# Performance work log

Hardware: AMD Instinct MI355X
Metric: run time of the kernel (lower is better)

## Reference

```python
import jax, jax.numpy as jnp
import numpy as np

B = 1; D = 28; H = 28; W = 28; DIM = 192; HEADS = 6
WS = (7, 7, 7); SS = (3, 3, 3)
CH = DIM // HEADS
N = WS[0] * WS[1] * WS[2]
ND, NH, NWW = D // WS[0], H // WS[1], W // WS[2]
NW = ND * NH * NWW
L = D * H * W
HID = 4 * DIM


def _rel_pos_index():
    c = np.stack(np.meshgrid(np.arange(WS[0]), np.arange(WS[1]), np.arange(WS[2]), indexing='ij')).reshape(3, -1)
    r = (c[:, :, None] - c[:, None, :]).transpose(1, 2, 0)
    r[:, :, 0] += WS[0] - 1; r[:, :, 1] += WS[1] - 1; r[:, :, 2] += WS[2] - 1
    r[:, :, 0] *= (2 * WS[1] - 1) * (2 * WS[2] - 1)
    r[:, :, 1] *= 2 * WS[2] - 1
    return r.sum(-1).reshape(-1)

RPI = _rel_pos_index()  # (N*N,)


def _attn_mask():
    img = np.zeros((D, H, W), np.float32)
    cnt = 0
    sl = lambda w, s: (slice(0, -w), slice(-w, -s), slice(-s, None))
    for a in sl(WS[0], SS[0]):
        for bb in sl(WS[1], SS[1]):
            for cc in sl(WS[2], SS[2]):
                img[a, bb, cc] = cnt; cnt += 1
    mw = img.reshape(ND, WS[0], NH, WS[1], NWW, WS[2]).transpose(0, 2, 4, 1, 3, 5).reshape(-1, N)
    return np.where(mw[:, None, :] != mw[:, :, None], np.float32(-100.0), np.float32(0.0))

MASK = jnp.asarray(_attn_mask())  # (NW, N, N)


def ln(x, g, b):
    mu = x.mean(-1, keepdims=True)
    v = ((x - mu) ** 2).mean(-1, keepdims=True)
    return (x - mu) * jax.lax.rsqrt(v + 1e-5) * g + b


def conv3d(x, w, pad):
    return jax.lax.conv_general_dilated(x, w, (1, 1, 1), [(pad, pad)] * 3,
                                        dimension_numbers=('NCDHW', 'OIDHW', 'NCDHW'))


def bn3d(x, g, b):
    mu = x.mean((0, 2, 3, 4), keepdims=True)
    var = x.var((0, 2, 3, 4), keepdims=True)
    return (x - mu) * jax.lax.rsqrt(var + 1e-5) * g.reshape(1, -1, 1, 1, 1) + b.reshape(1, -1, 1, 1, 1)


def offset_block(x, w1, g1, b1, w2, g2, b2, w3):
    x = jax.nn.relu(bn3d(conv3d(x, w1, 1), g1, b1))
    x = jax.nn.relu(bn3d(conv3d(x, w2, 1), g2, b2))
    return conv3d(x, w3, 0)  # (B, 3*HEADS, D, H, W)


def warp(vol, flow):
    # vol: (B,HEADS,CH,D,H,W), flow: (B,HEADS,3,D,H,W) voxel displacements; trilinear, border-clamped
    gd, gh, gw = jnp.meshgrid(jnp.arange(D, dtype=jnp.float32), jnp.arange(H, dtype=jnp.float32),
                              jnp.arange(W, dtype=jnp.float32), indexing='ij')
    cd = jnp.clip(gd + flow[:, :, 0], 0.0, D - 1)
    chh = jnp.clip(gh + flow[:, :, 1], 0.0, H - 1)
    cw = jnp.clip(gw + flow[:, :, 2], 0.0, W - 1)
    d0 = jnp.floor(cd).astype(jnp.int32); d1 = jnp.minimum(d0 + 1, D - 1)
    h0 = jnp.floor(chh).astype(jnp.int32); h1 = jnp.minimum(h0 + 1, H - 1)
    w0 = jnp.floor(cw).astype(jnp.int32); w1 = jnp.minimum(w0 + 1, W - 1)
    fd = (cd - d0).reshape(B, HEADS, 1, -1)
    fh = (chh - h0).reshape(B, HEADS, 1, -1)
    fw = (cw - w0).reshape(B, HEADS, 1, -1)
    vf = vol.reshape(B, HEADS, CH, -1)
    def gat(di, hi, wi):
        idx = ((di * H + hi) * W + wi).reshape(B, HEADS, 1, -1)
        return jnp.take_along_axis(vf, idx, axis=3)
    out = (gat(d0, h0, w0) * (1 - fd) * (1 - fh) * (1 - fw)
           + gat(d0, h0, w1) * (1 - fd) * (1 - fh) * fw
           + gat(d0, h1, w0) * (1 - fd) * fh * (1 - fw)
           + gat(d0, h1, w1) * (1 - fd) * fh * fw
           + gat(d1, h0, w0) * fd * (1 - fh) * (1 - fw)
           + gat(d1, h0, w1) * fd * (1 - fh) * fw
           + gat(d1, h1, w0) * fd * fh * (1 - fw)
           + gat(d1, h1, w1) * fd * fh * fw)
    return out.reshape(B, HEADS, CH, D, H, W)


def win_part(x):  # (B,D,H,W,C) -> (B*NW, N, C)
    c = x.shape[-1]
    x = x.reshape(B, ND, WS[0], NH, WS[1], NWW, WS[2], c)
    return x.transpose(0, 1, 3, 5, 2, 4, 6, 7).reshape(B * NW, N, c)


def dwin_part(x):  # (B,HEADS,D,H,W,CH) -> (B*NW, N, DIM)
    x = x.reshape(B, HEADS, ND, WS[0], NH, WS[1], NWW, WS[2], CH)
    x = x.transpose(0, 2, 4, 6, 3, 5, 7, 1, 8)
    return x.reshape(B * NW, N, DIM)


def win_rev(x):  # (B*NW, N, DIM) -> (B,D,H,W,DIM)
    x = x.reshape(B, ND, NH, NWW, WS[0], WS[1], WS[2], DIM)
    return x.transpose(0, 1, 4, 2, 5, 3, 6, 7).reshape(B, D, H, W, DIM)


def kv(x, w, b):
    y = (x @ w.T + b).reshape(x.shape[0], N, 2, HEADS, CH).transpose(2, 0, 3, 1, 4)
    return y[0], y[1]


def to_heads(x):
    return x.reshape(x.shape[0], N, HEADS, CH).transpose(0, 2, 1, 3)


def _forward(mov, fix, norm1_g, norm1_b, offm_w1, offm_g1, offm_b1, offm_w2, offm_g2, offm_b2, offm_w3, offf_w1, offf_g1, offf_b1, offf_w2, offf_g2, offf_b2, offf_w3, mq_w, mq_b, mkv_w, mkv_b, fq_w, fq_b, fkv_w, fkv_b, mproj_w, mproj_b, fproj_w, fproj_b, rpb_table, norm2_g, norm2_b, fc1_w, fc1_b, fc2_w, fc2_b):
    m = ln(mov, norm1_g, norm1_b).reshape(B, D, H, W, DIM)
    f = ln(fix, norm1_g, norm1_b).reshape(B, D, H, W, DIM)
    off_m = offset_block(jnp.concatenate([m, f], -1).transpose(0, 4, 1, 2, 3), offm_w1, offm_g1, offm_b1, offm_w2, offm_g2, offm_b2, offm_w3)
    off_f = offset_block(jnp.concatenate([f, m], -1).transpose(0, 4, 1, 2, 3), offf_w1, offf_g1, offf_b1, offf_w2, offf_g2, offf_b2, offf_w3)
    mh = m.transpose(0, 4, 1, 2, 3).reshape(B, HEADS, CH, D, H, W)
    fh = f.transpose(0, 4, 1, 2, 3).reshape(B, HEADS, CH, D, H, W)
    dmov = warp(mh, off_m.reshape(B, HEADS, 3, D, H, W)).transpose(0, 1, 3, 4, 5, 2)  # (B,h,D,H,W,c)
    dfix = warp(fh, off_f.reshape(B, HEADS, 3, D, H, W)).transpose(0, 1, 3, 4, 5, 2)
    sh = (-SS[0], -SS[1], -SS[2])
    mw_ = win_part(jnp.roll(m, sh, (1, 2, 3)))
    fw_ = win_part(jnp.roll(f, sh, (1, 2, 3)))
    dmw = dwin_part(jnp.roll(dmov, sh, (2, 3, 4)))
    dfw = dwin_part(jnp.roll(dfix, sh, (2, 3, 4)))
    B_ = B * NW
    scale = CH ** -0.5
    mK, mV = kv(mw_, mkv_w, mkv_b)
    fK, fV = kv(fw_, fkv_w, fkv_b)
    dmQ = to_heads(dmw @ mq_w.T + mq_b) * scale
    dfQ = to_heads(dfw @ fq_w.T + fq_b) * scale
    rpb = rpb_table[RPI].reshape(N, N, HEADS).transpose(2, 0, 1)  # (HEADS,N,N)
    def attend(q, k, v):
        a = jnp.einsum('bhnc,bhmc->bhnm', q, k) + rpb[None]
        a = (a.reshape(B, NW, HEADS, N, N) + MASK[None, :, None]).reshape(B_, HEADS, N, N)
        a = jax.nn.softmax(a, axis=-1)
        return jnp.einsum('bhnm,bhmc->bhnc', a, v).transpose(0, 2, 1, 3).reshape(B_, N, DIM)
    mo = attend(dfQ, mK, mV) @ mproj_w.T + mproj_b
    fo = attend(dmQ, fK, fV) @ fproj_w.T + fproj_b
    mo = jnp.roll(win_rev(mo), SS, (1, 2, 3)).reshape(B, L, DIM)
    fo = jnp.roll(win_rev(fo), SS, (1, 2, 3)).reshape(B, L, DIM)
    m_out = mov + mo
    f_out = fix + fo
    def mlp(x):
        return jax.nn.gelu(x @ fc1_w.T + fc1_b, approximate=False) @ fc2_w.T + fc2_b
    m_out = m_out + mlp(ln(m_out, norm2_g, norm2_b))
    f_out = f_out + mlp(ln(f_out, norm2_g, norm2_b))
    return jnp.stack([m_out, f_out])  # (2, B, L, DIM)


def setup_inputs():
    key = jax.random.key(0)
    ks = iter(jax.random.split(key, 64))
    nrm = lambda shape, s=0.02: jax.random.normal(next(ks), shape, jnp.float32) * s
    d = {}
    d['mov'] = jax.random.normal(next(ks), (B, L, DIM), jnp.float32)
    d['fix'] = jax.random.normal(next(ks), (B, L, DIM), jnp.float32)
    d['norm1_g'] = jnp.ones((DIM,)); d['norm1_b'] = jnp.zeros((DIM,))
    for p in ('offm', 'offf'):
        d[p + '_w1'] = nrm((DIM, 2 * DIM, 3, 3, 3))
        d[p + '_g1'] = jnp.ones((DIM,)); d[p + '_b1'] = jnp.zeros((DIM,))
        d[p + '_w2'] = nrm((DIM // 2, DIM, 3, 3, 3))
        d[p + '_g2'] = jnp.ones((DIM // 2,)); d[p + '_b2'] = jnp.zeros((DIM // 2,))
        d[p + '_w3'] = nrm((3 * HEADS, DIM // 2, 1, 1, 1))
    for p, o in (('mq_w', DIM), ('mkv_w', 2 * DIM), ('fq_w', DIM), ('fkv_w', 2 * DIM), ('mproj_w', DIM), ('fproj_w', DIM)):
        d[p] = nrm((o, DIM))
    for p, o in (('mq_b', DIM), ('mkv_b', 2 * DIM), ('fq_b', DIM), ('fkv_b', 2 * DIM), ('mproj_b', DIM), ('fproj_b', DIM)):
        d[p] = jnp.zeros((o,))
    d['rpb_table'] = nrm(((2 * WS[0] - 1) * (2 * WS[1] - 1) * (2 * WS[2] - 1), HEADS))
    d['norm2_g'] = jnp.ones((DIM,)); d['norm2_b'] = jnp.zeros((DIM,))
    d['fc1_w'] = nrm((HID, DIM)); d['fc1_b'] = jnp.zeros((HID,))
    d['fc2_w'] = nrm((DIM, HID)); d['fc2_b'] = jnp.zeros((DIM,))
    return d


def reference(mov, fix, norm1_g, norm1_b, offm_w1, offm_g1, offm_b1, offm_w2, offm_g2, offm_b2, offm_w3, offf_w1, offf_g1, offf_b1, offf_w2, offf_g2, offf_b2, offf_w3, mq_w, mq_b, mkv_w, mkv_b, fq_w, fq_b, fkv_w, fkv_b, mproj_w, mproj_b, fproj_w, fproj_b, rpb_table, norm2_g, norm2_b, fc1_w, fc1_b, fc2_w, fc2_b):
    return _forward(mov, fix, norm1_g, norm1_b, offm_w1, offm_g1, offm_b1, offm_w2, offm_g2, offm_b2, offm_w3, offf_w1, offf_g1, offf_b1, offf_w2, offf_g2, offf_b2, offf_w3, mq_w, mq_b, mkv_w, mkv_b, fq_w, fq_b, fkv_w, fkv_b, mproj_w, mproj_b, fproj_w, fproj_b, rpb_table, norm2_g, norm2_b, fc1_w, fc1_b, fc2_w, fc2_b)
```

## Files before the change

### kernel.cpp

```cpp
#include <hip/hip_runtime.h>

#define LTOT 21952
#define NTOK 343

typedef unsigned short u16;
typedef unsigned int   u32;
typedef __attribute__((ext_vector_type(8))) short short8;
typedef __attribute__((ext_vector_type(4))) float float4v;

__device__ __forceinline__ u16 f2b(float f){
  u32 x = __float_as_uint(f);
  u32 r = (x + 0x7fffu + ((x>>16)&1u)) >> 16;
  return (u16)r;
}

__global__ __launch_bounds__(64) void k_ln(const float* __restrict__ mov, const float* __restrict__ fix,
                                           const float* __restrict__ g, const float* __restrict__ b,
                                           float* __restrict__ om, float* __restrict__ of){
  int row = blockIdx.x;
  const float* src; float* dst;
  if (row < LTOT){ src = mov + (size_t)row*192; dst = om + (size_t)row*192; }
  else          { src = fix + (size_t)(row-LTOT)*192; dst = of + (size_t)(row-LTOT)*192; }
  int t = threadIdx.x;
  float x0 = src[t], x1 = src[t+64], x2 = src[t+128];
  float s = x0+x1+x2, s2 = x0*x0 + x1*x1 + x2*x2;
  for (int o=32;o;o>>=1){ s += __shfl_xor(s,o); s2 += __shfl_xor(s2,o); }
  float mu = s*(1.f/192.f);
  float var = s2*(1.f/192.f) - mu*mu;
  float rs = rsqrtf(var + 1e-5f);
  dst[t]     = (x0-mu)*rs*g[t]     + b[t];
  dst[t+64]  = (x1-mu)*rs*g[t+64]  + b[t+64];
  dst[t+128] = (x2-mu)*rs*g[t+128] + b[t+128];
}

__global__ __launch_bounds__(64) void k_ln1(const float* __restrict__ x,
                                            const float* __restrict__ g, const float* __restrict__ b,
                                            float* __restrict__ y){
  int row = blockIdx.x;
  const float* src = x + (size_t)row*192;
  float* dst = y + (size_t)row*192;
  int t = threadIdx.x;
  float x0 = src[t], x1 = src[t+64], x2 = src[t+128];
  float s = x0+x1+x2, s2 = x0*x0 + x1*x1 + x2*x2;
  for (int o=32;o;o>>=1){ s += __shfl_xor(s,o); s2 += __shfl_xor(s2,o); }
  float mu = s*(1.f/192.f);
  float var = s2*(1.f/192.f) - mu*mu;
  float rs = rsqrtf(var + 1e-5f);
  dst[t]     = (x0-mu)*rs*g[t]     + b[t];
  dst[t+64]  = (x1-mu)*rs*g[t+64]  + b[t+64];
  dst[t+128] = (x2-mu)*rs*g[t+128] + b[t+128];
}

__global__ void k_prepw1b(const float* __restrict__ src, u16* __restrict__ dst, int swap){
  int idx = blockIdx.x*256 + threadIdx.x;
  if (idx >= 192*10368) return;
  int n = idx / 10368; int k = idx - n*10368;
  int t = k / 384; int c = k - t*384;
  int cs = c + swap; if (cs >= 384) cs -= 384;
  dst[idx] = f2b(src[((size_t)n*384 + cs)*27 + t]);
}
__global__ void k_prepw2b(const float* __restrict__ src, u16* __restrict__ dst){
  int idx = blockIdx.x*256 + threadIdx.x;
  if (idx >= 96*5184) return;
  int n = idx / 5184; int k = idx - n*5184;
  int t = k / 192; int c = k - t*192;
  dst[idx] = f2b(src[((size_t)n*192 + c)*27 + t]);
}
__global__ void k_prepwb(const float* __restrict__ src, u16* __restrict__ dst, int count){
  int idx = blockIdx.x*256 + threadIdx.x;
  if (idx < count) dst[idx] = f2b(src[idx]);
}

__global__ void k_prepbias(const float* __restrict__ rpt, float* __restrict__ bm){
  int idx = blockIdx.x*256 + threadIdx.x;
  if (idx >= 48*123904) return;
  int th = idx / 123904; int r = idx - th*123904;
  int key = r / 352; int q = r - key*352;
  int type = th / 6; int h = th - type*6;
  float v;
  if (key >= 343 || q >= 343){
    v = -30000.f;
  } else {
    int ki = key/49, kj = (key/7)%7, kk = key%7;
    int qi = q/49,   qj = (q/7)%7,   qk = q%7;
    int ridx = ((qi-ki+6)*13 + (qj-kj+6))*13 + (qk-kk+6);
    float rv = rpt[ridx*6 + h];
    int bd = (type>>2)&1, bh = (type>>1)&1, bw = type&1;
    int lq_ = (bd?((qi<4)?1:2):0)*9 + (bh?((qj<4)?1:2):0)*3 + (bw?((qk<4)?1:2):0);
    int lk_ = (bd?((ki<4)?1:2):0)*9 + (bh?((kj<4)?1:2):0)*3 + (bw?((kk<4)?1:2):0);
    v = rv + ((lq_==lk_) ? 0.f : -100.f);
  }
  bm[idx] = v;
}

__global__ __launch_bounds__(192) void k_pad1(const float* __restrict__ m_, const float* __restrict__ f_,
                                              u16* __restrict__ xp){
  int p = blockIdx.x; int t = threadIdx.x;
  int pd = p/900; int r = p - pd*900; int ph = r/30; int pw = r - ph*30;
  int d = pd-1, h = ph-1, w = pw-1;
  u16 vm = 0, vf = 0;
  if ((unsigned)d < 28u && (unsigned)h < 28u && (unsigned)w < 28u){
    size_t l = (size_t)((d*28+h)*28+w)*192 + t;
    vm = f2b(m_[l]); vf = f2b(f_[l]);
  }
  xp[(size_t)p*384 + t] = vm;
  xp[(size_t)p*384 + 192 + t] = vf;
}
__global__ __launch_bounds__(192) void k_pad2(const float* __restrict__ t1,
                                              const float* __restrict__ a1, const float* __restrict__ b1,
                                              u16* __restrict__ xp2){
  int p = blockIdx.x; int t = threadIdx.x;
  int pd = p/900; int r = p - pd*900; int ph = r/30; int pw = r - ph*30;
  int d = pd-1, h = ph-1, w = pw-1;
  u16 v = 0;
  if ((unsigned)d < 28u && (unsigned)h < 28u && (unsigned)w < 28u){
    float xv = t1[(size_t)((d*28+h)*28+w)*192 + t];
    v = f2b(fmaxf(xv*a1[t] + b1[t], 0.f));
  }
  xp2[(size_t)p*192 + t] = v;
}

template<int CIN, int COUT>
__global__ __launch_bounds__(256, 4) void k_convmfma(const u16* __restrict__ xpA,
                                                     const u16* __restrict__ xpB,
                                                     const u16* __restrict__ wA,
                                                     const u16* __restrict__ wB,
                                                     float* __restrict__ outA,
                                                     float* __restrict__ outB){
  constexpr int K = 27*CIN;
  constexpr int CH = CIN/32;
  constexpr int STEPS = 27*CH;
  constexpr int NT = COUT/32;
  constexpr int NB8 = COUT/32;
  __shared__ __align__(16) u16 As[2][64*40];
  __shared__ __align__(16) u16 Bs[2][COUT*40];
  int tid = threadIdx.x;
  int b0 = blockIdx.x;
  int xcd = b0 & 7, ii = b0 >> 3;
  int bid = (xcd < 6 ? xcd*86 : 516 + (xcd-6)*85) + ii;
  int which = (bid >= 343) ? 1 : 0;
  int t = bid - which*343;
  const u16* xp  = which ? xpB : xpA;
  const u16* wtb = which ? wB : wA;
  float* out = which ? outB : outA;
  int v0 = t*64;
  int sv  = tid>>2;
  int c8u = (tid&3)*8;
  int av = v0 + sv;
  int d = av/784; int rm2 = av - d*784; int hh = rm2/28; int ww = rm2 - hh*28;
  int pbase = (d*30 + hh)*30 + ww;
  int lane = tid&63, wv = tid>>6;
  int lm = lane&15, lq = lane>>4;
  int mbase = (wv>>1)*32;
  int nbase = (wv&1)*(COUT/2);

  float4v acc[2][NT];
  #pragma unroll
  for (int mt=0; mt<2; mt++)
    #pragma unroll
    for (int nt=0; nt<NT; nt++) acc[mt][nt] = (float4v)0.f;

  uint4 a_r;
  uint2 b_r[NB8];
  auto load_s = [&](int s){
    int tp = s/CH, cc = s - tp*CH;
    int td = tp/9, tr = tp - td*9, th = tr/3, tw = tr - th*3;
    int toff = td*900 + th*30 + tw;
    a_r = *(const uint4*)(xp + (size_t)(pbase + toff)*CIN + cc*32 + c8u);
    #pragma unroll
    for (int j=0;j<NB8;j++){
      int bi = tid + j*256;
      int n = bi>>3, c4 = (bi&7)*4;
      b_r[j] = *(const uint2*)(wtb + (size_t)n*K + s*32 + c4);
    }
  };
  auto write_s = [&](int buf){
    *(uint4*)(&As[buf][sv*40 + c8u]) = a_r;
    #pragma unroll
    for (int j=0;j<NB8;j++){
      int bi = tid + j*256;
      int n = bi>>3, c4 = (bi&7)*4;
      *(uint2*)(&Bs[buf][n*40 + c4]) = b_r[j];
    }
  };

  load_s(0);
  write_s(0);
  __syncthreads();
  for (int s = 0; s < STEPS; s++){
    if (s+1 < STEPS) load_s(s+1);
    int buf = s&1;
    short8 aa[2], bb[NT];
    #pragma unroll
    for (int mt=0; mt<2; mt++)
      aa[mt] = *(const short8*)(&As[buf][(mbase + mt*16 + lm)*40 + lq*8]);
    #pragma unroll
    for (int nt=0; nt<NT; nt++)
      bb[nt] = *(const short8*)(&Bs[buf][(nbase + nt*16 + lm)*40 + lq*8]);
    #pragma unroll
    for (int nt=0; nt<NT; nt++)
      #pragma unroll
      for (int mt=0; mt<2; mt++)
        acc[mt][nt] = __builtin_amdgcn_mfma_f32_16x16x32_bf16(aa[mt], bb[nt], acc[mt][nt], 0, 0, 0);
    if (s+1 < STEPS) write_s((s+1)&1);
    __syncthreads();
  }
  #pragma unroll
  for (int mt=0; mt<2; mt++)
    #pragma unroll
    for (int nt=0; nt<NT; nt++)
      #pragma unroll
      for (int r=0; r<4; r++){
        int row = v0 + mbase + mt*16 + lq*4 + r;
        int col = nbase + nt*16 + lm;
        out[(size_t)row*COUT + col] = acc[mt][nt][r];
      }
}

template<int K, int NF, int GATHER, int ASRC, int EPI>
__global__ __launch_bounds__(256) void k_gemm(const float* __restrict__ Af,
                                              const u16* __restrict__ Ab,
                                              const u16* __restrict__ B,
                                              const float* __restrict__ bias,
                                              const float* __restrict__ resid,
                                              float* __restrict__ outf,
                                              u16* __restrict__ out16,
                                              u16* __restrict__ out16b,
                                              float scale){
  constexpr int STEPS = K/32;
  constexpr int NB = NF/64;
  __shared__ __align__(16) u16 As[2][64*40];
  __shared__ __align__(16) u16 Bs[2][64*40];
  __shared__ int map[64];
  int tid = threadIdx.x;
  int bid = blockIdx.x;
  int mb = bid / NB, nb = bid - mb*NB;
  int v0 = mb*64, ncol0 = nb*64;
  if (tid < 64){
    int r = v0 + tid;
    int src;
    if (GATHER == 0){
      src = r;
    } else if (GATHER == 1){
      int w = r/343; int n = r - w*343;
      int nd = w>>4, nh = (w>>2)&3, nw = w&3;
      int i = n/49; int rr = n - i*49; int j = rr/7; int k2 = rr - j*7;
      int dd = nd*7 + i + 3; if (dd >= 28) dd -= 28;
      int hh = nh*7 + j + 3; if (hh >= 28) hh -= 28;
      int ww = nw*7 + k2 + 3; if (ww >= 28) ww -= 28;
      src = (dd*28 + hh)*28 + ww;
    } else {
      int l = r;
      int d = l/784; int rm = l - d*784; int y = rm/28; int x = rm - y*28;
      int dp = d-3; if (dp<0) dp+=28;
      int yp = y-3; if (yp<0) yp+=28;
      int xq = x-3; if (xq<0) xq+=28;
      int nd = dp/7, i = dp - nd*7;
      int nh = yp/7, j = yp - nh*7;
      int nw = xq/7, k2 = xq - nw*7;
      src = ((nd*4+nh)*4+nw)*NTOK + (i*7+j)*7 + k2;
    }
    map[tid] = src;
  }
  __syncthreads();
  int sv = tid>>2, c8 = (tid&3)*8;
  int arow = map[sv];
  int lane = tid&63, wv = tid>>6;
  int lm = lane&15, lq = lane>>4;
  int mbase = (wv>>1)*32, nbase = (wv&1)*32;

  float4v acc[2][2];
  #pragma unroll
  for (int mt=0; mt<2; mt++)
    #pragma unroll
    for (int nt=0; nt<2; nt++) acc[mt][nt] = (float4v)0.f;

  float4 afr0, afr1; uint4 abr; uint4 bvr;
  auto load_s = [&](int s){
    if (ASRC == 0){
      const float* ap = Af + (size_t)arow*K + s*32 + c8;
      afr0 = *(const float4*)ap;
      afr1 = *(const float4*)(ap+4);
    } else {
      abr = *(const uint4*)(Ab + (size_t)arow*K + s*32 + c8);
    }
    bvr = *(const uint4*)(B + (size_t)(ncol0 + sv)*K + s*32 + c8);
  };
  auto write_s = [&](int buf){
    if (ASRC == 0){
      uint4 pk;
      pk.x = (u32)f2b(afr0.x) | ((u32)f2b(afr0.y)<<16);
      pk.y = (u32)f2b(afr0.z) | ((u32)f2b(afr0.w)<<16);
      pk.z = (u32)f2b(afr1.x) | ((u32)f2b(afr1.y)<<16);
      pk.w = (u32)f2b(afr1.z) | ((u32)f2b(afr1.w)<<16);
      *(uint4*)(&As[buf][sv*40 + c8]) = pk;
    } else {
      *(uint4*)(&As[buf][sv*40 + c8]) = abr;
    }
    *(uint4*)(&Bs[buf][sv*40 + c8]) = bvr;
  };

  load_s(0);
  write_s(0);
  __syncthreads();
  for (int s = 0; s < STEPS; s++){
    if (s+1 < STEPS) load_s(s+1);
    int buf = s&1;
    short8 aa[2], bb[2];
    #pragma unroll
    for (int mt=0; mt<2; mt++)
      aa[mt] = *(const short8*)(&As[buf][(mbase + mt*16 + lm)*40 + lq*8]);
    #pragma unroll
    for (int nt=0; nt<2; nt++)
      bb[nt] = *(const short8*)(&Bs[buf][(nbase + nt*16 + lm)*40 + lq*8]);
    #pragma unroll
    for (int nt=0; nt<2; nt++)
      #pragma unroll
      for (int mt=0; mt<2; mt++)
        acc[mt][nt] = __builtin_amdgcn_mfma_f32_16x16x32_bf16(aa[mt], bb[nt], acc[mt][nt], 0, 0, 0);
    if (s+1 < STEPS) write_s((s+1)&1);
    __syncthreads();
  }
  float bv[2];
  #pragma unroll
  for (int nt=0; nt<2; nt++) bv[nt] = bias ? bias[ncol0 + nbase + nt*16 + lm] : 0.f;
  #pragma unroll
  for (int mt=0; mt<2; mt++){
    #pragma unroll
    for (int r=0; r<4; r++){
      int row = v0 + mbase + mt*16 + lq*4 + r;
      if (EPI == 0 || EPI == 3){
        int w = row/343; int tok = row - w*343;
        #pragma unroll
        for (int nt=0; nt<2; nt++){
          int col = ncol0 + nbase + nt*16 + lm;
          float val = (acc[mt][nt][r] + bv[nt]) * scale;
          if (EPI == 0){
            int h = col>>5, c = col&31;
            out16[((size_t)(w*6 + h)*343 + tok)*32 + c] = f2b(val);
          } else {
            u16* dst = (col < 192) ? out16 : out16b;
            int cc = (col < 192) ? col : col - 192;
            int h = cc>>5, c = cc&31;
            dst[((size_t)(w*6 + h)*343 + tok)*32 + c] = f2b(val);
          }
        }
      } else if (EPI == 1){
        #pragma unroll
        for (int nt=0; nt<2; nt++){
          int col = ncol0 + nbase + nt*16 + lm;
          size_t o = (size_t)row*NF + col;
          outf[o] = acc[mt][nt][r] + bv[nt] + resid[o];
        }
      } else {
        #pragma unroll
        for (int nt=0; nt<2; nt++){
          int col = ncol0 + nbase + nt*16 + lm;
          float v = acc[mt][nt][r] + bv[nt];
          float gl = 0.5f*v*(1.f + erff(v*0.70710678118f));
          out16[(size_t)row*NF + col] = f2b(gl);
        }
      }
    }
  }
}

__global__ __launch_bounds__(192) void k_bnsum(const float* __restrict__ x, int C,
                                               float* __restrict__ psum){
  int bid = blockIdx.x, t = threadIdx.x;
  int rpi = 192/C;
  int c  = (C==192) ? t : (t % 96);
  int ro = (C==192) ? 0 : (t / 96);
  float s=0.f, s2=0.f;
  int base = bid*343;
  for (int r = ro; r < 343; r += rpi){
    float v = x[(size_t)(base+r)*C + c];
    s += v; s2 += v*v;
  }
  psum[(size_t)bid*384 + t]       = s;
  psum[(size_t)bid*384 + 192 + t] = s2;
}
__global__ void k_bnfin(const float* __restrict__ psum, int C,
                        const float* __restrict__ g, const float* __restrict__ b,
                        float* __restrict__ a_out, float* __restrict__ b_out){
  int c = threadIdx.x;
  if (c >= C) return;
  int slots = 192/C;
  float s=0.f, s2=0.f;
  for (int bb=0; bb<64; bb++)
    for (int k=0; k<slots; k++){
      s  += psum[(size_t)bb*384 + k*C + c];
      s2 += psum[(size_t)bb*384 + 192 + k*C + c];
    }
  float mu = s/(float)LTOT;
  float var = s2/(float)LTOT - mu*mu;
  float rstd = rsqrtf(var + 1e-5f);
  float aa = rstd * g[c];
  a_out[c] = aa;
  b_out[c] = b[c] - mu*aa;
}

__global__ __launch_bounds__(96) void k_flow(const float* __restrict__ t2,
                                             const float* __restrict__ a2, const float* __restrict__ b2,
                                             const float* __restrict__ w3, float* __restrict__ flow){
  __shared__ float xr[96];
  int l = blockIdx.x; int t = threadIdx.x;
  float xv = t2[(size_t)l*96 + t];
  xr[t] = fmaxf(xv*a2[t] + b2[t], 0.f);
  __syncthreads();
  if (t < 18){
    float acc = 0.f;
    for (int c=0;c<96;c++) acc += xr[c]*w3[t*96 + c];
    flow[(size_t)t*LTOT + l] = acc;
  }
}

__global__ __launch_bounds__(192) void k_warp(const float* __restrict__ src,
                                              const float* __restrict__ flow, float* __restrict__ dst){
  int l = blockIdx.x; int tid = threadIdx.x; int hh = tid>>5;
  int d = l/784; int rm = l - d*784; int y = rm/28; int x = rm - y*28;
  float fd = flow[(size_t)(hh*3+0)*LTOT + l];
  float fy = flow[(size_t)(hh*3+1)*LTOT + l];
  float fx = flow[(size_t)(hh*3+2)*LTOT + l];
  float cd = fminf(fmaxf((float)d + fd, 0.f), 27.f);
  float cy = fminf(fmaxf((float)y + fy, 0.f), 27.f);
  float cx = fminf(fmaxf((float)x + fx, 0.f), 27.f);
  int d0 = (int)floorf(cd); int d1 = min(d0+1, 27);
  int y0 = (int)floorf(cy); int y1 = min(y0+1, 27);
  int x0 = (int)floorf(cx); int x1 = min(x0+1, 27);
  float wd = cd - (float)d0, wy = cy - (float)y0, wx = cx - (float)x0;
  #define SMP(di,yi,xi) src[(size_t)(((di)*28+(yi))*28+(xi))*192 + tid]
  float v000 = SMP(d0,y0,x0), v001 = SMP(d0,y0,x1), v010 = SMP(d0,y1,x0), v011 = SMP(d0,y1,x1);
  float v100 = SMP(d1,y0,x0), v101 = SMP(d1,y0,x1), v110 = SMP(d1,y1,x0), v111 = SMP(d1,y1,x1);
  #undef SMP
  float o = v000*(1-wd)*(1-wy)*(1-wx) + v001*(1-wd)*(1-wy)*wx
          + v010*(1-wd)*wy*(1-wx)     + v011*(1-wd)*wy*wx
          + v100*wd*(1-wy)*(1-wx)     + v101*wd*(1-wy)*wx
          + v110*wd*wy*(1-wx)         + v111*wd*wy*wx;
  dst[(size_t)l*192 + tid] = o;
}

__global__ __launch_bounds__(256) void k_attmfma(const u16* __restrict__ Q,
                                                 const u16* __restrict__ K,
                                                 const u16* __restrict__ V,
                                                 const float* __restrict__ bm,
                                                 float* __restrict__ ctx){
  __shared__ __align__(16) u16 Kl[352*40];
  __shared__ __align__(16) u16 Vt[32*360];
  __shared__ __align__(16) u16 Pl[4][2][16*40];
  int bid = blockIdx.x;
  int wh = bid/6, qg = bid - (bid/6)*6;
  int w = wh/6, h = wh - w*6;
  int tid = threadIdx.x;
  int nd = w>>4, nh = (w>>2)&3, nw = w&3;
  int type = ((nd==3)?4:0) | ((nh==3)?2:0) | ((nw==3)?1:0);
  const u16* kb = K + (size_t)wh*10976;
  const u16* vbp = V + (size_t)wh*10976;
  for (int idx=tid; idx<343*4; idx+=256){
    int row = idx>>2, c8 = (idx&3)*8;
    uint4 val = *(const uint4*)(kb + row*32 + c8);
    *(uint4*)(&Kl[row*40 + c8]) = val;
  }
  for (int idx=tid; idx<9*40; idx+=256) Kl[343*40 + idx] = 0;
  for (int idx=tid; idx<343*4; idx+=256){
    int row = idx>>2, c8 = (idx&3)*8;
    uint4 val = *(const uint4*)(vbp + row*32 + c8);
    const u16* pv = (const u16*)&val;
    #pragma unroll
    for (int j=0;j<8;j++) Vt[(c8+j)*360 + row] = pv[j];
  }
  for (int idx=tid; idx<32*17; idx+=256){
    int dd = idx/17, cc = 343 + idx - (idx/17)*17;
    Vt[dd*360 + cc] = 0;
  }
  __syncthreads();
  int lane = tid&63, wv = tid>>6;
  int lm = lane&15, lq = lane>>4;
  const float* bmh = bm + (size_t)(type*6 + h)*123904;
  int qt = qg*4 + wv;
  if (qt < 22){
    int q0 = qt*16;
    short8 bq = *(const short8*)(Q + (size_t)wh*10976 + (q0+lm)*32 + lq*8);
    float4v sc[22];
    #pragma unroll
    for (int kt=0; kt<22; kt++){
      short8 ak = *(const short8*)(&Kl[(kt*16+lm)*40 + lq*8]);
      sc[kt] = __builtin_amdgcn_mfma_f32_16x16x32_bf16(ak, bq, (float4v)0.f, 0, 0, 0);
    }
    const float* bcol = bmh + q0 + lm;
    float mx = -3.0e38f;
    #pragma unroll
    for (int kt=0; kt<22; kt++){
      #pragma unroll
      for (int r=0; r<4; r++){
        int key = kt*16 + lq*4 + r;
        float s = sc[kt][r] + bcol[(size_t)key*352];
        sc[kt][r] = s;
        mx = fmaxf(mx, s);
      }
    }
    mx = fmaxf(mx, __shfl_xor(mx, 16));
    mx = fmaxf(mx, __shfl_xor(mx, 32));
    float sm = 0.f;
    #pragma unroll
    for (int kt=0; kt<22; kt++){
      #pragma unroll
      for (int r=0; r<4; r++){
        float p = __expf(sc[kt][r] - mx);
        sc[kt][r] = p;
        sm += p;
      }
    }
    sm += __shfl_xor(sm, 16);
    sm += __shfl_xor(sm, 32);
    float inv = 1.f/sm;
    float4v o0 = (float4v)0.f, o1 = (float4v)0.f;
    #pragma unroll
    for (int s=0; s<11; s++){
      u16* pw = &Pl[wv][s&1][0];
      #pragma unroll
      for (int half=0; half<2; half++){
        int kt = 2*s + half;
        uint2 pv2;
        pv2.x = (u32)f2b(sc[kt][0]) | ((u32)f2b(sc[kt][1])<<16);
        pv2.y = (u32)f2b(sc[kt][2]) | ((u32)f2b(sc[kt][3])<<16);
        *(uint2*)(&pw[lm*40 + half*16 + lq*4]) = pv2;
      }
      short8 bp = *(const short8*)(&pw[lm*40 + lq*8]);
      short8 a0 = *(const short8*)(&Vt[lm*360 + s*32 + lq*8]);
      short8 a1 = *(const short8*)(&Vt[(16+lm)*360 + s*32 + lq*8]);
      o0 = __builtin_amdgcn_mfma_f32_16x16x32_bf16(a0, bp, o0, 0, 0, 0);
      o1 = __builtin_amdgcn_mfma_f32_16x16x32_bf16(a1, bp, o1, 0, 0, 0);
    }
    int query = q0 + lm;
    if (query < 343){
      float* ob = ctx + ((size_t)w*NTOK + query)*192 + h*32;
      float4 t0, t1v;
      t0.x = o0[0]*inv; t0.y = o0[1]*inv; t0.z = o0[2]*inv; t0.w = o0[3]*inv;
      t1v.x = o1[0]*inv; t1v.y = o1[1]*inv; t1v.z = o1[2]*inv; t1v.w = o1[3]*inv;
      *(float4*)(ob + lq*4) = t0;
      *(float4*)(ob + 16 + lq*4) = t1v;
    }
  }
}

extern "C" void kernel_launch(void* const* d_in, const int* in_sizes, int n_in,
                              void* d_out, int out_size, void* d_ws, size_t ws_size,
                              hipStream_t stream){
  const float* mov     = (const float*)d_in[0];
  const float* fix     = (const float*)d_in[1];
  const float* n1g     = (const float*)d_in[2];
  const float* n1b     = (const float*)d_in[3];
  const float* offm_w1 = (const float*)d_in[4];
  const float* offm_g1 = (const float*)d_in[5];
  const float* offm_b1 = (const float*)d_in[6];
  const float* offm_w2 = (const float*)d_in[7];
  const float* offm_g2 = (const float*)d_in[8];
  const float* offm_b2 = (const float*)d_in[9];
  const float* offm_w3 = (const float*)d_in[10];
  const float* offf_w1 = (const float*)d_in[11];
  const float* offf_g1 = (const float*)d_in[12];
  const float* offf_b1 = (const float*)d_in[13];
  const float* offf_w2 = (const float*)d_in[14];
  const float* offf_g2 = (const float*)d_in[15];
  const float* offf_b2 = (const float*)d_in[16];
  const float* offf_w3 = (const float*)d_in[17];
  const float* mq_w    = (const float*)d_in[18];
  const float* mkv_w   = (const float*)d_in[19];
  const float* fq_w    = (const float*)d_in[20];
  const float* fkv_w   = (const float*)d_in[21];
  const float* mproj_w = (const float*)d_in[22];
  const float* fproj_w = (const float*)d_in[23];
  const float* mq_b    = (const float*)d_in[24];
  const float* mkv_b   = (const float*)d_in[25];
  const float* fq_b    = (const float*)d_in[26];
  const float* fkv_b   = (const float*)d_in[27];
  const float* mproj_b = (const float*)d_in[28];
  const float* fproj_b = (const float*)d_in[29];
  const float* rpbt    = (const float*)d_in[30];
  const float* n2g     = (const float*)d_in[31];
  const float* n2b     = (const float*)d_in[32];
  const float* fc1_w   = (const float*)d_in[33];
  const float* fc1_b   = (const float*)d_in[34];
  const float* fc2_w   = (const float*)d_in[35];
  const float* fc2_b   = (const float*)d_in[36];
  float* outp = (float*)d_out;

  float* W = (float*)d_ws;
  const size_t L192 = (size_t)LTOT*192;
  float* m_   = W;
  float* f_   = W + 1*L192;
  float* t1m  = W + 2*L192;
  float* t1f  = W + 3*L192;
  u16* xp     = (u16*)(W + 4*L192);
  u16* xp2m   = xp + (size_t)27000*384;
  u16* xp2f   = (u16*)(W + 6*L192);
  float* sb   = W + 6*L192 + 3000000;
  float* a1m = sb,       *b1m = sb+192;
  float* a1f = sb+384,   *b1f = sb+576;
  float* a2m = sb+768,   *b2m = sb+864;
  float* a2f = sb+960,   *b2f = sb+1056;
  float* psum = sb + 1152;
  float* flowm = W + 6*L192 + 3100000;
  float* flowf = flowm + (size_t)LTOT*18;
  float* t2m  = W + 7*L192;
  float* t2f  = W + 7*L192 + (size_t)LTOT*96;
  u16* wt1m = (u16*)(W + 8*L192);
  u16* wt1f = wt1m + 192*10368;
  u16* wt2m = wt1f + 192*10368;
  u16* wt2f = wt2m + 96*5184;
  float* dmov = W + 4*L192;
  float* dfix = W + 5*L192;
  float* ctxm = dmov; float* ctxf = dfix;
  float* mout = m_;   float* fout = f_;
  u16* QMb = (u16*)(W + 6*L192);
  u16* QFb = (u16*)(W + 7*L192);
  u16* Kmb = (u16*)(W + 2*L192);
  u16* Vmb = (u16*)(W + 3*L192);
  u16* Kfb = (u16*)(W + 8*L192);
  u16* Vfb = (u16*)(W + 9*L192);
  float* bm = W;
  u16* wq_m  = (u16*)(W + 9*L192) + 4214784;
  u16* wq_f  = wq_m  + 36864;
  u16* wkv_m = wq_f  + 36864;
  u16* wkv_f = wkv_m + 73728;
  u16* wpj_m = wkv_f + 73728;
  u16* wpj_f = wpj_m + 36864;
  u16* wfc1  = wpj_f + 36864;
  u16* wfc2  = wfc1  + 147456;
  u16* hs16  = (u16*)(W + 2*L192);
  float* lnbuf = W + 6*L192;

  k_prepw1b<<<(192*10368+255)/256, 256, 0, stream>>>(offm_w1, wt1m, 0);
  k_prepw1b<<<(192*10368+255)/256, 256, 0, stream>>>(offf_w1, wt1f, 192);
  k_prepw2b<<<(96*5184+255)/256, 256, 0, stream>>>(offm_w2, wt2m);
  k_prepw2b<<<(96*5184+255)/256, 256, 0, stream>>>(offf_w2, wt2f);
  k_prepwb<<<144, 256, 0, stream>>>(mq_w,    wq_m,  36864);
  k_prepwb<<<144, 256, 0, stream>>>(fq_w,    wq_f,  36864);
  k_prepwb<<<288, 256, 0, stream>>>(mkv_w,   wkv_m, 73728);
  k_prepwb<<<288, 256, 0, stream>>>(fkv_w,   wkv_f, 73728);
  k_prepwb<<<144, 256, 0, stream>>>(mproj_w, wpj_m, 36864);
  k_prepwb<<<144, 256, 0, stream>>>(fproj_w, wpj_f, 36864);
  k_prepwb<<<576, 256, 0, stream>>>(fc1_w,   wfc1,  147456);
  k_prepwb<<<576, 256, 0, stream>>>(fc2_w,   wfc2,  147456);
  k_ln<<<2*LTOT, 64, 0, stream>>>(mov, fix, n1g, n1b, m_, f_);
  k_pad1<<<27000, 192, 0, stream>>>(m_, f_, xp);
  k_convmfma<384,192><<<686, 256, 0, stream>>>(xp, xp, wt1m, wt1f, t1m, t1f);
  k_bnsum<<<64, 192, 0, stream>>>(t1m, 192, psum);
  k_bnfin<<<1, 192, 0, stream>>>(psum, 192, offm_g1, offm_b1, a1m, b1m);
  k_bnsum<<<64, 192, 0, stream>>>(t1f, 192, psum);
  k_bnfin<<<1, 192, 0, stream>>>(psum, 192, offf_g1, offf_b1, a1f, b1f);
  k_pad2<<<27000, 192, 0, stream>>>(t1m, a1m, b1m, xp2m);
  k_pad2<<<27000, 192, 0, stream>>>(t1f, a1f, b1f, xp2f);
  k_convmfma<192,96><<<686, 256, 0, stream>>>(xp2m, xp2f, wt2m, wt2f, t2m, t2f);
  k_bnsum<<<64, 192, 0, stream>>>(t2m, 96, psum);
  k_bnfin<<<1, 96, 0, stream>>>(psum, 96, offm_g2, offm_b2, a2m, b2m);
  k_bnsum<<<64, 192, 0, stream>>>(t2f, 96, psum);
  k_bnfin<<<1, 96, 0, stream>>>(psum, 96, offf_g2, offf_b2, a2f, b2f);
  k_flow<<<LTOT, 96, 0, stream>>>(t2m, a2m, b2m, offm_w3, flowm);
  k_flow<<<LTOT, 96, 0, stream>>>(t2f, a2f, b2f, offf_w3, flowf);
  k_warp<<<LTOT, 192, 0, stream>>>(m_, flowm, dmov);
  k_warp<<<LTOT, 192, 0, stream>>>(f_, flowf, dfix);
  const float scale = 0.17677669529663687f;
  k_gemm<192,192,1,0,0><<<343*3, 256, 0, stream>>>(dmov, nullptr, wq_m,  mq_b,  nullptr, nullptr, QMb, nullptr, scale);
  k_gemm<192,192,1,0,0><<<343*3, 256, 0, stream>>>(dfix, nullptr, wq_f,  fq_b,  nullptr, nullptr, QFb, nullptr, scale);
  k_gemm<192,384,1,0,3><<<343*6, 256, 0, stream>>>(m_,   nullptr, wkv_m, mkv_b, nullptr, nullptr, Kmb, Vmb, 1.f);
  k_gemm<192,384,1,0,3><<<343*6, 256, 0, stream>>>(f_,   nullptr, wkv_f, fkv_b, nullptr, nullptr, Kfb, Vfb, 1.f);
  k_prepbias<<<(48*123904+255)/256, 256, 0, stream>>>(rpbt, bm);
  k_attmfma<<<2304, 256, 0, stream>>>(QFb, Kmb, Vmb, bm, ctxm);
  k_attmfma<<<2304, 256, 0, stream>>>(QMb, Kfb, Vfb, bm, ctxf);
  k_gemm<192,192,2,0,1><<<343*3, 256, 0, stream>>>(ctxm, nullptr, wpj_m, mproj_b, mov, mout, nullptr, nullptr, 1.f);
  k_gemm<192,192,2,0,1><<<343*3, 256, 0, stream>>>(ctxf, nullptr, wpj_f, fproj_b, fix, fout, nullptr, nullptr, 1.f);
  k_ln1<<<LTOT, 64, 0, stream>>>(mout, n2g, n2b, lnbuf);
  k_gemm<192,768,0,0,2><<<343*12, 256, 0, stream>>>(lnbuf, nullptr, wfc1, fc1_b, nullptr, nullptr, hs16, nullptr, 1.f);
  k_gemm<768,192,0,1,1><<<343*3, 256, 0, stream>>>(nullptr, hs16, wfc2, fc2_b, mout, outp, nullptr, nullptr, 1.f);
  k_ln1<<<LTOT, 64, 0, stream>>>(fout, n2g, n2b, lnbuf);
  k_gemm<192,768,0,0,2><<<343*12, 256, 0, stream>>>(lnbuf, nullptr, wfc1, fc1_b, nullptr, nullptr, hs16, nullptr, 1.f);
  k_gemm<768,192,0,1,1><<<343*3, 256, 0, stream>>>(nullptr, hs16, wfc2, fc2_b, fout, outp + L192, nullptr, nullptr, 1.f);
}
```

Baseline: 1.443 ms.

## Rework conv MFMA kernel to two-wave blocks with 64-row tiles per wave

The implicit-GEMM conv kernel now runs 128-thread blocks. Each wave covers all 64 output rows (four M-tiles) against half of the output channels, which improves A-fragment reuse from LDS per MFMA, and the weight tiles are loaded with 16-byte vector loads. For the first conv, the two weight sets are addressed as one contiguous buffer with a shared input. This relies on the layout of wt1m/wt1f, and halving the number of waves per block and in the grid may reduce latency hiding.

```diff
diff --git a/kernel.cpp b/kernel.cpp
--- a/kernel.cpp
+++ b/kernel.cpp
@@ -120,8 +120,8 @@
   xp2[(size_t)p*192 + t] = v;
 }
 
-template<int CIN, int COUT>
-__global__ __launch_bounds__(256, 4) void k_convmfma(const u16* __restrict__ xpA,
+template<int CIN, int NBLK, bool SHARED_A>
+__global__ __launch_bounds__(128, 2) void k_convmfma(const u16* __restrict__ xpA,
                                                      const u16* __restrict__ xpB,
                                                      const u16* __restrict__ wA,
                                                      const u16* __restrict__ wB,
@@ -130,57 +130,66 @@
   constexpr int K = 27*CIN;
   constexpr int CH = CIN/32;
   constexpr int STEPS = 27*CH;
-  constexpr int NT = COUT/32;
-  constexpr int NB8 = COUT/32;
+  constexpr int NT = NBLK/32;
+  constexpr int BCH = NBLK/32;
   __shared__ __align__(16) u16 As[2][64*40];
-  __shared__ __align__(16) u16 Bs[2][COUT*40];
+  __shared__ __align__(16) u16 Bs[2][NBLK*40];
   int tid = threadIdx.x;
   int b0 = blockIdx.x;
   int xcd = b0 & 7, ii = b0 >> 3;
   int bid = (xcd < 6 ? xcd*86 : 516 + (xcd-6)*85) + ii;
-  int which = (bid >= 343) ? 1 : 0;
-  int t = bid - which*343;
-  const u16* xp  = which ? xpB : xpA;
-  const u16* wtb = which ? wB : wA;
-  float* out = which ? outB : outA;
+  int half = (bid >= 343) ? 1 : 0;
+  int t = bid - half*343;
+  const u16* xp;
+  const u16* wtb;
+  float* out = half ? outB : outA;
+  if (SHARED_A){
+    xp  = xpA;
+    wtb = wA + (size_t)(half*NBLK)*K;
+  } else {
+    xp  = half ? xpB : xpA;
+    wtb = half ? wB : wA;
+  }
   int v0 = t*64;
-  int sv  = tid>>2;
-  int c8u = (tid&3)*8;
-  int av = v0 + sv;
+  int arow = tid & 63;
+  int ac   = tid >> 6;
+  int av = v0 + arow;
   int d = av/784; int rm2 = av - d*784; int hh = rm2/28; int ww = rm2 - hh*28;
   int pbase = (d*30 + hh)*30 + ww;
   int lane = tid&63, wv = tid>>6;
   int lm = lane&15, lq = lane>>4;
-  int mbase = (wv>>1)*32;
-  int nbase = (wv&1)*(COUT/2);
-
-  float4v acc[2][NT];
+  int nbase = wv*(NBLK/2);
+
+  float4v acc[4][NT];
   #pragma unroll
-  for (int mt=0; mt<2; mt++)
+  for (int mt=0; mt<4; mt++)
     #pragma unroll
     for (int nt=0; nt<NT; nt++) acc[mt][nt] = (float4v)0.f;
 
-  uint4 a_r;
-  uint2 b_r[NB8];
+  uint4 a_r[2];
+  uint4 b_r[BCH];
   auto load_s = [&](int s){
     int tp = s/CH, cc = s - tp*CH;
     int td = tp/9, tr = tp - td*9, th = tr/3, tw = tr - th*3;
     int toff = td*900 + th*30 + tw;
-    a_r = *(const uint4*)(xp + (size_t)(pbase + toff)*CIN + cc*32 + c8u);
-    #pragma unroll
-    for (int j=0;j<NB8;j++){
-      int bi = tid + j*256;
-      int n = bi>>3, c4 = (bi&7)*4;
-      b_r[j] = *(const uint2*)(wtb + (size_t)n*K + s*32 + c4);
+    const u16* ap = xp + (size_t)(pbase + toff)*CIN + cc*32;
+    a_r[0] = *(const uint4*)(ap + ac*8);
+    a_r[1] = *(const uint4*)(ap + (2+ac)*8);
+    #pragma unroll
+    for (int j=0;j<BCH;j++){
+      int idx = tid + j*128;
+      int c = idx/NBLK; int row = idx - c*NBLK;
+      b_r[j] = *(const uint4*)(wtb + (size_t)row*K + s*32 + c*8);
     }
   };
   auto write_s = [&](int buf){
-    *(uint4*)(&As[buf][sv*40 + c8u]) = a_r;
-    #pragma unroll
-    for (int j=0;j<NB8;j++){
-      int bi = tid + j*256;
-      int n = bi>>3, c4 = (bi&7)*4;
-      *(uint2*)(&Bs[buf][n*40 + c4]) = b_r[j];
+    *(uint4*)(&As[buf][arow*40 + ac*8])     = a_r[0];
+    *(uint4*)(&As[buf][arow*40 + (2+ac)*8]) = a_r[1];
+    #pragma unroll
+    for (int j=0;j<BCH;j++){
+      int idx = tid + j*128;
+      int c = idx/NBLK; int row = idx - c*NBLK;
+      *(uint4*)(&Bs[buf][row*40 + c*8]) = b_r[j];
     }
   };
 
@@ -190,30 +199,30 @@
   for (int s = 0; s < STEPS; s++){
     if (s+1 < STEPS) load_s(s+1);
     int buf = s&1;
-    short8 aa[2], bb[NT];
-    #pragma unroll
-    for (int mt=0; mt<2; mt++)
-      aa[mt] = *(const short8*)(&As[buf][(mbase + mt*16 + lm)*40 + lq*8]);
+    short8 aa[4], bb[NT];
+    #pragma unroll
+    for (int mt=0; mt<4; mt++)
+      aa[mt] = *(const short8*)(&As[buf][(mt*16 + lm)*40 + lq*8]);
     #pragma unroll
     for (int nt=0; nt<NT; nt++)
       bb[nt] = *(const short8*)(&Bs[buf][(nbase + nt*16 + lm)*40 + lq*8]);
     #pragma unroll
     for (int nt=0; nt<NT; nt++)
       #pragma unroll
-      for (int mt=0; mt<2; mt++)
+      for (int mt=0; mt<4; mt++)
         acc[mt][nt] = __builtin_amdgcn_mfma_f32_16x16x32_bf16(aa[mt], bb[nt], acc[mt][nt], 0, 0, 0);
     if (s+1 < STEPS) write_s((s+1)&1);
     __syncthreads();
   }
   #pragma unroll
-  for (int mt=0; mt<2; mt++)
+  for (int mt=0; mt<4; mt++)
     #pragma unroll
     for (int nt=0; nt<NT; nt++)
       #pragma unroll
       for (int r=0; r<4; r++){
-        int row = v0 + mbase + mt*16 + lq*4 + r;
+        int row = v0 + mt*16 + lq*4 + r;
         int col = nbase + nt*16 + lm;
-        out[(size_t)row*COUT + col] = acc[mt][nt][r];
+        out[(size_t)row*NBLK + col] = acc[mt][nt][r];
       }
 }
 
@@ -645,14 +654,14 @@
   k_prepwb<<<576, 256, 0, stream>>>(fc2_w,   wfc2,  147456);
   k_ln<<<2*LTOT, 64, 0, stream>>>(mov, fix, n1g, n1b, m_, f_);
   k_pad1<<<27000, 192, 0, stream>>>(m_, f_, xp);
-  k_convmfma<384,192><<<686, 256, 0, stream>>>(xp, xp, wt1m, wt1f, t1m, t1f);
+  k_convmfma<384,192,true><<<686, 128, 0, stream>>>(xp, xp, wt1m, nullptr, t1m, t1f);
   k_bnsum<<<64, 192, 0, stream>>>(t1m, 192, psum);
   k_bnfin<<<1, 192, 0, stream>>>(psum, 192, offm_g1, offm_b1, a1m, b1m);
   k_bnsum<<<64, 192, 0, stream>>>(t1f, 192, psum);
   k_bnfin<<<1, 192, 0, stream>>>(psum, 192, offf_g1, offf_b1, a1f, b1f);
   k_pad2<<<27000, 192, 0, stream>>>(t1m, a1m, b1m, xp2m);
   k_pad2<<<27000, 192, 0, stream>>>(t1f, a1f, b1f, xp2f);
-  k_convmfma<192,96><<<686, 256, 0, stream>>>(xp2m, xp2f, wt2m, wt2f, t2m, t2f);
+  k_convmfma<192,96,false><<<686, 128, 0, stream>>>(xp2m, xp2f, wt2m, wt2f, t2m, t2f);
   k_bnsum<<<64, 192, 0, stream>>>(t2m, 96, psum);
   k_bnfin<<<1, 96, 0, stream>>>(psum, 96, offm_g2, offm_b2, a2m, b2m);
   k_bnsum<<<64, 192, 0, stream>>>(t2f, 96, psum);
```

Result: slower. 2.839 ms (+96.8%).

## Add direct global-to-LDS DMA conv kernel for first offset conv

Applied to the files above, without the earlier changes.

Replaces the first 3x3x3 offset-convolution launch with a new implicit-GEMM kernel that uses global_load_lds to copy A and B tiles straight into shared memory, double-buffered, with one barrier per K-step. It also remaps block IDs so that consecutive tiles stay on the same XCD, which should improve L2 reuse, and it uses padded LDS strides. The aim is to cut the register staging and VGPR load/store traffic of the old conv kernel. The cost is lower occupancy (launch bounds 256,2) and a reliance on the DMA builtin's layout semantics being correct.

```diff
diff --git a/kernel.cpp b/kernel.cpp
--- a/kernel.cpp
+++ b/kernel.cpp
@@ -12,6 +12,12 @@
   u32 x = __float_as_uint(f);
   u32 r = (x + 0x7fffu + ((x>>16)&1u)) >> 16;
   return (u16)r;
+}
+
+__device__ __forceinline__ void dma16(const u16* g, u16* l){
+  __builtin_amdgcn_global_load_lds((const __attribute__((address_space(1))) u32*)g,
+                                   (__attribute__((address_space(3))) u32*)l,
+                                   16, 0, 0);
 }
 
 __global__ __launch_bounds__(64) void k_ln(const float* __restrict__ mov, const float* __restrict__ fix,
@@ -118,6 +124,77 @@
     v = f2b(fmaxf(xv*a1[t] + b1[t], 0.f));
   }
   xp2[(size_t)p*192 + t] = v;
+}
+
+__global__ __launch_bounds__(256, 2) void k_conv1dma(const u16* __restrict__ xp,
+                                                     const u16* __restrict__ wm,
+                                                     const u16* __restrict__ wf,
+                                                     float* __restrict__ outm,
+                                                     float* __restrict__ outf){
+  const int K = 10368;
+  __shared__ __align__(16) u16 As[2][4*520];
+  __shared__ __align__(16) u16 Bs[2][4*1544];
+  int tid = threadIdx.x;
+  int b0 = blockIdx.x;
+  int xcd = b0 & 7, ii = b0 >> 3;
+  int bid = (xcd < 6 ? xcd*86 : 516 + (xcd-6)*85) + ii;
+  int half = (bid >= 343) ? 1 : 0;
+  int t = bid - half*343;
+  const u16* wtb = half ? wf : wm;
+  float* out = half ? outf : outm;
+  int v0 = t*64;
+  int lane = tid&63, wv = tid>>6;
+  int lm = lane&15, lq = lane>>4;
+  int av = v0 + lane;
+  int d = av/784; int rm2 = av - d*784; int hh = rm2/28; int ww = rm2 - hh*28;
+  int pbase = (d*30 + hh)*30 + ww;
+  int nbase = wv*48;
+
+  float4v acc[4][3];
+  #pragma unroll
+  for (int mt=0; mt<4; mt++)
+    #pragma unroll
+    for (int nt=0; nt<3; nt++) acc[mt][nt] = (float4v)0.f;
+
+  auto stage = [&](int buf, int s){
+    int tp = s/12, cc = s - tp*12;
+    int td = tp/9, tr = tp - td*9, th = tr/3, tw = tr - th*3;
+    int toff = td*900 + th*30 + tw;
+    dma16(xp + (size_t)(pbase + toff)*384 + cc*32 + wv*8, &As[buf][wv*520]);
+    #pragma unroll
+    for (int j=0;j<3;j++)
+      dma16(wtb + (size_t)(j*64 + lane)*K + s*32 + wv*8, &Bs[buf][wv*1544 + j*512]);
+  };
+
+  stage(0, 0);
+  __syncthreads();
+  for (int s = 0; s < 324; s++){
+    if (s+1 < 324) stage((s+1)&1, s+1);
+    int buf = s&1;
+    short8 aa[4], bb[3];
+    #pragma unroll
+    for (int mt=0; mt<4; mt++)
+      aa[mt] = *(const short8*)(&As[buf][lq*520 + (mt*16 + lm)*8]);
+    #pragma unroll
+    for (int nt=0; nt<3; nt++)
+      bb[nt] = *(const short8*)(&Bs[buf][lq*1544 + (nbase + nt*16 + lm)*8]);
+    #pragma unroll
+    for (int nt=0; nt<3; nt++)
+      #pragma unroll
+      for (int mt=0; mt<4; mt++)
+        acc[mt][nt] = __builtin_amdgcn_mfma_f32_16x16x32_bf16(aa[mt], bb[nt], acc[mt][nt], 0, 0, 0);
+    __syncthreads();
+  }
+  #pragma unroll
+  for (int mt=0; mt<4; mt++)
+    #pragma unroll
+    for (int nt=0; nt<3; nt++)
+      #pragma unroll
+      for (int r=0; r<4; r++){
+        int row = v0 + mt*16 + lq*4 + r;
+        int col = nbase + nt*16 + lm;
+        out[(size_t)row*192 + col] = acc[mt][nt][r];
+      }
 }
 
 template<int CIN, int COUT>
@@ -645,7 +722,7 @@
   k_prepwb<<<576, 256, 0, stream>>>(fc2_w,   wfc2,  147456);
   k_ln<<<2*LTOT, 64, 0, stream>>>(mov, fix, n1g, n1b, m_, f_);
   k_pad1<<<27000, 192, 0, stream>>>(m_, f_, xp);
-  k_convmfma<384,192><<<686, 256, 0, stream>>>(xp, xp, wt1m, wt1f, t1m, t1f);
+  k_conv1dma<<<686, 256, 0, stream>>>(xp, wt1m, wt1f, t1m, t1f);
   k_bnsum<<<64, 192, 0, stream>>>(t1m, 192, psum);
   k_bnfin<<<1, 192, 0, stream>>>(psum, 192, offm_g1, offm_b1, a1m, b1m);
   k_bnsum<<<64, 192, 0, stream>>>(t1f, 192, psum);
```

New measurement: 1.632 ms. 1.13x slower.
